# Performance work log

Measured on AMD Instinct MI355X. Metric: run time of the kernel, lower is better.

Reference implementation:

```python
import jax, jax.numpy as jnp
import numpy as np

DELAY = 4
SKIP = 2
NF = 8
HS = 256
EPS = 1e-5


def setup_inputs() -> dict:
    key = jax.random.key(0)
    ks = jax.random.split(key, 11)
    B, NP, NO, T = 16, 512, 512, 2048
    predictor = jax.random.normal(ks[0], (B, NP, T), dtype=jnp.float32)
    to_order = jax.random.normal(ks[1], (B, NO, T), dtype=jnp.float32)
    trilinear = jax.random.normal(ks[2], (NF, NO, NP), dtype=jnp.float32) / np.float32(np.sqrt(NP * NO))
    w_o = jax.random.normal(ks[3], (HS, NO), dtype=jnp.float32) / np.float32(np.sqrt(NO))
    b_o = jax.random.normal(ks[4], (HS,), dtype=jnp.float32) * 0.01
    w_p = jax.random.normal(ks[5], (HS, NP), dtype=jnp.float32) / np.float32(np.sqrt(NP))
    b_p = jax.random.normal(ks[6], (HS,), dtype=jnp.float32) * 0.01
    bn_gamma = jnp.ones((HS,), dtype=jnp.float32)
    bn_beta = jnp.zeros((HS,), dtype=jnp.float32)
    w_out = jax.random.normal(ks[7], (NF, HS), dtype=jnp.float32) / np.float32(np.sqrt(HS))
    b_out = jax.random.normal(ks[8], (NF,), dtype=jnp.float32) * 0.01
    return {"predictor": predictor, "to_order": to_order, "trilinear": trilinear,
            "w_o": w_o, "b_o": b_o, "w_p": w_p, "b_p": b_p,
            "bn_gamma": bn_gamma, "bn_beta": bn_beta, "w_out": w_out, "b_out": b_out}


def reference(predictor, to_order, trilinear, w_o, b_o, w_p, b_p, bn_gamma, bn_beta, w_out, b_out):
    B, NP, T = predictor.shape
    NO = to_order.shape[1]
    tot_latency = DELAY + SKIP * (NF - 1)
    T_r = T - tot_latency
    pred = predictor[:, :, :T_r]          # (B, np, Tr)
    too = to_order[:, :, DELAY:]          # (B, no, T - delay)
    # predictor_product[b,k,t,m] = sum_p pred[b,p,t] * trilinear[k,m,p]
    pp = jnp.einsum('bpt,kmp->bktm', pred, trilinear)           # (B, nf, Tr, no)
    win = jnp.stack([too[:, :, j * SKIP: j * SKIP + T_r] for j in range(NF)], axis=1)  # (B, nf, no, Tr)
    inner = jnp.einsum('bjmt,bktm->bjkt', win, pp)              # (B, nf, nf, Tr)
    # conv1d (kernel 1) heads
    o_proj = jnp.einsum('hm,bmt->bht', w_o, too) + b_o[None, :, None]    # (B, hs, T - delay)
    p_proj = jnp.einsum('hp,bpt->bht', w_p, pred) + b_p[None, :, None]   # (B, hs, Tr)
    o_win = jnp.stack([o_proj[:, :, j * SKIP: j * SKIP + T_r] for j in range(NF)], axis=1)  # (B, nf, hs, Tr)
    h = jax.nn.relu(o_win + p_proj[:, None])                    # (B, nf, hs, Tr)
    # BatchNorm1d (training-mode batch stats) over (B*nf, hs, Tr): stats over axes (0,1,3)
    mean = h.mean(axis=(0, 1, 3), keepdims=True)
    var = h.var(axis=(0, 1, 3), keepdims=True)
    h = (h - mean) * jax.lax.rsqrt(var + EPS) * bn_gamma[None, None, :, None] + bn_beta[None, None, :, None]
    head = jnp.einsum('kh,bjht->bjkt', w_out, h) + b_out[None, None, :, None]
    inner = inner + head
    log_probs = jax.nn.log_softmax(inner, axis=2)               # (B, nf, nf, Tr)
    correct = jnp.einsum('bjjt->bjt', log_probs)                # diagonal j == k
    return correct.mean(axis=2).mean(axis=0)                    # (nf,)
```

## Files before the change

### kernel.cpp

```cpp
#include <hip/hip_runtime.h>
#include <math.h>

constexpr int B_  = 16;
constexpr int NP_ = 512;
constexpr int NO_ = 512;
constexpr int T_  = 2048;
constexpr int NF_ = 8;
constexpr int HS_ = 256;
constexpr int TR_ = 2030;
constexpr int TO_ = 2044;
constexpr int OPLD_ = 2048;
constexpr float EPS_ = 1e-5f;

typedef short bf16x8 __attribute__((ext_vector_type(8)));
typedef float f32x16 __attribute__((ext_vector_type(16)));

__device__ __forceinline__ unsigned short f2bf(float f) {
  union { float f; unsigned int u; } v; v.f = f;
  unsigned int r = v.u + 0x7fffu + ((v.u >> 16) & 1u);
  return (unsigned short)(r >> 16);
}
__device__ __forceinline__ float bf2f(unsigned short u) {
  union { unsigned int u; float f; } v; v.u = ((unsigned int)u) << 16;
  return v.f;
}

typedef const __attribute__((address_space(1))) unsigned int* gas_u32;
typedef __attribute__((address_space(3))) unsigned int* las_u32;
__device__ __forceinline__ void gl16(const void* g, void* l) {
  __builtin_amdgcn_global_load_lds((gas_u32)g, (las_u32)l, 16, 0, 0);
}


__global__ __launch_bounds__(256) void transpose_cvt(
    const float* __restrict__ in, unsigned short* __restrict__ outb) {
  __shared__ float tile[64][65];
  const int c0 = blockIdx.x * 64;
  const int r0 = blockIdx.y * 64;
  const int b  = blockIdx.z;
  const float* ib = in + (size_t)b * 512 * 2048;
  unsigned short* ob = outb + (size_t)b * 2048 * 512;
  for (int i = threadIdx.x; i < 64 * 16; i += 256) {
    const int r = i >> 4, c4 = (i & 15) * 4;
    float4 v = *(const float4*)(ib + (size_t)(r0 + r) * 2048 + c0 + c4);
    tile[r][c4 + 0] = v.x; tile[r][c4 + 1] = v.y;
    tile[r][c4 + 2] = v.z; tile[r][c4 + 3] = v.w;
  }
  __syncthreads();
  for (int i = threadIdx.x; i < 64 * 8; i += 256) {
    const int c = i >> 3, r8 = (i & 7) * 8;
    unsigned int pk[4];
    #pragma unroll
    for (int e = 0; e < 4; ++e)
      pk[e] = (unsigned int)f2bf(tile[r8 + 2 * e][c]) |
              ((unsigned int)f2bf(tile[r8 + 2 * e + 1][c]) << 16);
    *(uint4*)(ob + (size_t)(c0 + c) * 512 + r0 + r8) = *(uint4*)pk;
  }
}

__global__ __launch_bounds__(256) void cvt_bf16(
    const float* __restrict__ in, unsigned short* __restrict__ out, int n) {
  const int i = (blockIdx.x * 256 + threadIdx.x) * 4;
  if (i < n) {
    float4 v = *(const float4*)(in + i);
    ushort4 o; o.x = f2bf(v.x); o.y = f2bf(v.y); o.z = f2bf(v.z); o.w = f2bf(v.w);
    *(ushort4*)(out + i) = o;
  }
}

__global__ __launch_bounds__(256, 2) void proj_mfma(
    const unsigned short* __restrict__ Wbf,
    const unsigned short* __restrict__ Xt,
    const float* __restrict__ bias,
    unsigned short* __restrict__ out,
    int Tlen, int toff) {
  __shared__ char smem[65536];
  char* const Ab[2] = { smem, smem + 16384 };
  char* const Bb[2] = { smem + 32768, smem + 49152 };
  const int tid = threadIdx.x;
  const int l = tid & 63, wv = tid >> 6;
  const int h = l >> 5, tl = l & 31;
  const int mq = wv >> 1, tq = wv & 1;
  const int t0 = blockIdx.x * 128;
  const int m0 = blockIdx.y * 128;
  const int b  = blockIdx.z;
  const unsigned short* Xb = Xt + (size_t)b * T_ * 512;

  int aSrc[4], bSrc[4], ldsO[4];
  #pragma unroll
  for (int i = 0; i < 4; ++i) {
    const int q = (wv << 8) + (i << 6) + l;
    const int r = q >> 3, c8s = (q & 7) ^ (r & 7);
    aSrc[i] = (m0 + r) * 512 + (c8s << 3);
    const int row = min(t0 + toff + r, T_ - 1);
    bSrc[i] = row * 512 + (c8s << 3);
    ldsO[i] = ((wv << 8) + (i << 6)) << 4;
  }

  f32x16 acc[2][2];
  #pragma unroll
  for (int i = 0; i < 2; ++i)
    #pragma unroll
    for (int jj = 0; jj < 2; ++jj)
      #pragma unroll
      for (int e = 0; e < 16; ++e) acc[i][jj][e] = 0.f;

  #pragma unroll
  for (int i = 0; i < 4; ++i) gl16(Wbf + aSrc[i], Ab[0] + ldsO[i]);
  #pragma unroll
  for (int i = 0; i < 4; ++i) gl16(Xb + bSrc[i], Bb[0] + ldsO[i]);
  asm volatile("s_waitcnt vmcnt(0)" ::: "memory");
  __builtin_amdgcn_s_barrier();

  #pragma unroll
  for (int ps = 0; ps < 8; ++ps) {
    const int cb = ps & 1;
    if (ps < 7) {
      const int p0 = (ps + 1) << 6;
      #pragma unroll
      for (int i = 0; i < 4; ++i) gl16(Wbf + p0 + aSrc[i], Ab[cb ^ 1] + ldsO[i]);
      #pragma unroll
      for (int i = 0; i < 4; ++i) gl16(Xb + p0 + bSrc[i], Bb[cb ^ 1] + ldsO[i]);
    }
    const unsigned short* As = (const unsigned short*)Ab[cb];
    const unsigned short* Bs = (const unsigned short*)Bb[cb];
    #pragma unroll
    for (int s = 0; s < 4; ++s) {
      const int k8 = 2 * s + h;
      bf16x8 af[2], bfr[2];
      #pragma unroll
      for (int mt = 0; mt < 2; ++mt) {
        const int rm = 64 * mq + 32 * mt + tl;
        af[mt] = *(const bf16x8*)(As + rm * 64 + ((k8 ^ (rm & 7)) << 3));
      }
      #pragma unroll
      for (int nt = 0; nt < 2; ++nt) {
        const int rt = 64 * tq + 32 * nt + tl;
        bfr[nt] = *(const bf16x8*)(Bs + rt * 64 + ((k8 ^ (rt & 7)) << 3));
      }
      #pragma unroll
      for (int mt = 0; mt < 2; ++mt)
        #pragma unroll
        for (int nt = 0; nt < 2; ++nt)
          acc[mt][nt] = __builtin_amdgcn_mfma_f32_32x32x16_bf16(
              af[mt], bfr[nt], acc[mt][nt], 0, 0, 0);
    }
    asm volatile("s_waitcnt vmcnt(0)" ::: "memory");
    __builtin_amdgcn_s_barrier();
  }
  #pragma unroll
  for (int mt = 0; mt < 2; ++mt)
    #pragma unroll
    for (int nt = 0; nt < 2; ++nt)
      #pragma unroll
      for (int r = 0; r < 16; ++r) {
        const int hs = m0 + 64 * mq + 32 * mt + (r & 3) + 8 * (r >> 2) + 4 * h;
        const int t  = t0 + 64 * tq + 32 * nt + tl;
        if (t < Tlen)
          out[((size_t)b * HS_ + hs) * OPLD_ + t] = f2bf(acc[mt][nt][r] + bias[hs]);
      }
}

__global__ __launch_bounds__(256, 2) void inner_mfma(
    const unsigned short* __restrict__ pred_t,
    const unsigned short* __restrict__ too_t,
    const unsigned short* __restrict__ tri_bf,
    float* __restrict__ inner) {
  __shared__ char smem[69632];
  char* const Pb[2] = { smem, smem + 16384 };
  char* const Tb[2] = { smem + 32768, smem + 40960 };
  char* const TOO   = smem + 49152;
  const int tid = threadIdx.x;
  const int l = tid & 63, wv = tid >> 6;
  const int h = l >> 5, tl = l & 31;
  const int t0 = blockIdx.x * 128;
  const int kf = blockIdx.y;
  const int b  = blockIdx.z;
  const unsigned short* predB = pred_t + (size_t)b * T_ * NP_;
  const unsigned short* tooB  = too_t  + (size_t)b * T_ * NO_;
  const unsigned short* triK  = tri_bf + (size_t)kf * NO_ * NP_;

  int pSrc[4], pLds[4];
  #pragma unroll
  for (int i = 0; i < 4; ++i) {
    const int q = (wv << 8) + (i << 6) + l;
    const int r = q >> 3, c8s = (q & 7) ^ (r & 7);
    pSrc[i] = (t0 + r) * NP_ + (c8s << 3);
    pLds[i] = ((wv << 8) + (i << 6)) << 4;
  }
  int tSrc[2], tLds[2];
  #pragma unroll
  for (int i = 0; i < 2; ++i) {
    const int q = (wv << 7) + (i << 6) + l;
    const int r = q >> 3, c8s = (q & 7) ^ (r & 7);
    tSrc[i] = r * NP_ + (c8s << 3);
    tLds[i] = ((wv << 7) + (i << 6)) << 4;
  }
  int oSrc[5], oLds[5];
  #pragma unroll
  for (int i = 0; i < 5; ++i) {
    const int q = wv * 320 + (i << 6) + l;
    const int r = q >> 3, c8s = (q & 7) ^ (r & 7);
    const int row = min(t0 + r, T_ - 1);
    oSrc[i] = row * NO_ + (c8s << 3);
    oLds[i] = (wv * 320 + (i << 6)) << 4;
  }

  f32x16 Sacc[2];
  #pragma unroll
  for (int ct = 0; ct < 2; ++ct)
    #pragma unroll
    for (int e = 0; e < 16; ++e) Sacc[ct][e] = 0.f;

  for (int mc = 0; mc < 8; ++mc) {
    const int m0 = mc << 6;
    const int mOff = m0 * NP_;
    __builtin_amdgcn_s_barrier();
    #pragma unroll
    for (int i = 0; i < 5; ++i) gl16(tooB + m0 + oSrc[i], TOO + oLds[i]);
    #pragma unroll
    for (int i = 0; i < 4; ++i) gl16(predB + pSrc[i], Pb[0] + pLds[i]);
    #pragma unroll
    for (int i = 0; i < 2; ++i) gl16(triK + mOff + tSrc[i], Tb[0] + tLds[i]);
    asm volatile("s_waitcnt vmcnt(0)" ::: "memory");
    __builtin_amdgcn_s_barrier();

    f32x16 Qacc[2];
    #pragma unroll
    for (int mt = 0; mt < 2; ++mt)
      #pragma unroll
      for (int e = 0; e < 16; ++e) Qacc[mt][e] = 0.f;

    #pragma unroll
    for (int ps = 0; ps < 8; ++ps) {
      const int cb = ps & 1;
      if (ps < 7) {
        const int p0 = (ps + 1) << 6;
        #pragma unroll
        for (int i = 0; i < 4; ++i) gl16(predB + p0 + pSrc[i], Pb[cb ^ 1] + pLds[i]);
        #pragma unroll
        for (int i = 0; i < 2; ++i) gl16(triK + mOff + p0 + tSrc[i], Tb[cb ^ 1] + tLds[i]);
      }
      const unsigned short* predS = (const unsigned short*)Pb[cb];
      const unsigned short* triS  = (const unsigned short*)Tb[cb];
      #pragma unroll
      for (int s = 0; s < 4; ++s) {
        const int k8 = 2 * s + h;
        const int rb = (wv << 5) + tl;
        const bf16x8 bp = *(const bf16x8*)(predS + rb * 64 + ((k8 ^ (rb & 7)) << 3));
        #pragma unroll
        for (int mt = 0; mt < 2; ++mt) {
          const int rm = (mt << 5) + tl;
          const bf16x8 at = *(const bf16x8*)(triS + rm * 64 + ((k8 ^ (rm & 7)) << 3));
          Qacc[mt] = __builtin_amdgcn_mfma_f32_32x32x16_bf16(at, bp, Qacc[mt], 0, 0, 0);
        }
      }
      asm volatile("s_waitcnt vmcnt(0)" ::: "memory");
      __builtin_amdgcn_s_barrier();
    }
    unsigned short* QSw = (unsigned short*)(Pb[0] + (wv << 12));
    #pragma unroll
    for (int mt = 0; mt < 2; ++mt)
      #pragma unroll
      for (int rp = 0; rp < 8; ++rp) {
        const int r = rp << 1;
        const int m = (mt << 5) + (r & 3) + ((r >> 2) << 3) + (h << 2);
        const int c8 = m >> 3, ml = m & 7;
        const int rX = (tl & 24) | ((tl ^ c8) & 7);
        const unsigned int pk = (unsigned int)f2bf(Qacc[mt][r]) |
                                ((unsigned int)f2bf(Qacc[mt][r + 1]) << 16);
        *(unsigned int*)(QSw + (((c8 << 5) + rX) << 3) + ml) = pk;
      }
    const unsigned short* tooS = (const unsigned short*)TOO;
    #pragma unroll
    for (int s = 0; s < 4; ++s) {
      const int k8 = 2 * s + h;
      const int rqX = (tl & 24) | ((tl ^ k8) & 7);
      const bf16x8 bq = *(const bf16x8*)(QSw + (((k8 << 5) + rqX) << 3));
      #pragma unroll
      for (int ct = 0; ct < 2; ++ct) {
        const int rr = (wv << 5) + (ct << 5) + tl;
        const bf16x8 atoo = *(const bf16x8*)(tooS + rr * 64 + ((k8 ^ (rr & 7)) << 3));
        Sacc[ct] = __builtin_amdgcn_mfma_f32_32x32x16_bf16(atoo, bq, Sacc[ct], 0, 0, 0);
      }
    }
  }
  __syncthreads();
  float* SW = (float*)smem + (wv << 11);
  #pragma unroll
  for (int ct = 0; ct < 2; ++ct)
    #pragma unroll
    for (int r = 0; r < 16; ++r) {
      const int cc = (ct << 5) + (r & 3) + ((r >> 2) << 3) + (h << 2);
      SW[(cc << 5) + tl] = Sacc[ct][r];
    }
  const int tglob = t0 + (wv << 5) + tl;
  if (tglob < TR_) {
    #pragma unroll
    for (int jj = 0; jj < 4; ++jj) {
      const int j = (jj << 1) + h;
      const float v = SW[((tl + 4 + 2 * j) << 5) + tl];
      inner[(((size_t)b * NF_ + j) * NF_ + kf) * TR_ + tglob] = v;
    }
  }
}

__global__ __launch_bounds__(256) void bn_stats(
    const unsigned short* __restrict__ op, const unsigned short* __restrict__ pp,
    float* __restrict__ partials) {
  const int hh = blockIdx.x, b = blockIdx.y;
  const unsigned short* oprow = op + ((size_t)b * HS_ + hh) * OPLD_;
  const unsigned short* pprow = pp + ((size_t)b * HS_ + hh) * OPLD_;
  float s = 0.f, s2 = 0.f;
  for (int t = threadIdx.x; t < TR_; t += 256) {
    const float pv = bf2f(pprow[t]);
    #pragma unroll
    for (int j = 0; j < NF_; ++j) {
      float r = bf2f(oprow[t + 2 * j]) + pv;
      r = fmaxf(r, 0.f);
      s += r; s2 += r * r;
    }
  }
  __shared__ float red[256], red2[256];
  red[threadIdx.x] = s; red2[threadIdx.x] = s2;
  __syncthreads();
  for (int st = 128; st > 0; st >>= 1) {
    if (threadIdx.x < st) {
      red[threadIdx.x]  += red[threadIdx.x + st];
      red2[threadIdx.x] += red2[threadIdx.x + st];
    }
    __syncthreads();
  }
  if (threadIdx.x == 0) {
    partials[b * HS_ + hh]            = red[0];
    partials[B_ * HS_ + b * HS_ + hh] = red2[0];
  }
}

__global__ __launch_bounds__(256) void bn_finalize(
    const float* __restrict__ partials, const float* __restrict__ gamma,
    const float* __restrict__ beta, const float* __restrict__ w_out,
    const float* __restrict__ b_out, float* __restrict__ w_eff,
    float* __restrict__ cvec) {
  const int hh = threadIdx.x;
  float s = 0.f, s2 = 0.f;
  for (int b = 0; b < B_; ++b) {
    s  += partials[b * HS_ + hh];
    s2 += partials[B_ * HS_ + b * HS_ + hh];
  }
  const float cnt  = (float)B_ * NF_ * TR_;
  const float mean = s / cnt;
  const float var  = s2 / cnt - mean * mean;
  const float scale = gamma[hh] * rsqrtf(var + EPS_);
  const float shift = beta[hh] - mean * scale;
  #pragma unroll
  for (int k = 0; k < NF_; ++k) w_eff[k * HS_ + hh] = w_out[k * HS_ + hh] * scale;
  __shared__ float red[256];
  for (int k = 0; k < NF_; ++k) {
    red[hh] = w_out[k * HS_ + hh] * shift;
    __syncthreads();
    for (int st = 128; st > 0; st >>= 1) {
      if (hh < st) red[hh] += red[hh + st];
      __syncthreads();
    }
    if (hh == 0) cvec[k] = b_out[k] + red[0];
    __syncthreads();
  }
}

__global__ __launch_bounds__(256) void head_final(
    const unsigned short* __restrict__ op, const unsigned short* __restrict__ pp,
    const float* __restrict__ w_eff, const float* __restrict__ cvec,
    const float* __restrict__ inner, float* __restrict__ part3) {
  __shared__ float opS[288 * 20];
  __shared__ float ppS[256 * 20];
  __shared__ float weS[8][256];
  __shared__ float red[4][5];
  const int tid = threadIdx.x;
  const int t0 = blockIdx.x * 256;
  const int b  = blockIdx.y;
  const int jh = blockIdx.z;
  for (int i = tid; i < 8 * 256; i += 256) weS[i >> 8][i & 255] = w_eff[i];
  float acc[4][8] = {};
  const unsigned short* opb = op + (size_t)b * HS_ * OPLD_;
  const unsigned short* ppb = pp + (size_t)b * HS_ * OPLD_;
  for (int hc = 0; hc < 16; ++hc) {
    const int h0 = hc << 4;
    __syncthreads();
    for (int idx = tid; idx < 576; idx += 256) {
      const int r = idx / 36, cc = (idx - r * 36) << 3;
      const int g = min(t0 + cc, OPLD_ - 8);
      uint4 v = *(const uint4*)(opb + (size_t)(h0 + r) * OPLD_ + g);
      #pragma unroll
      for (int e = 0; e < 4; ++e) {
        const unsigned int u = (&v.x)[e];
        opS[(cc + 2 * e) * 20 + r]     = bf2f((unsigned short)(u & 0xffffu));
        opS[(cc + 2 * e + 1) * 20 + r] = bf2f((unsigned short)(u >> 16));
      }
    }
    for (int idx = tid; idx < 512; idx += 256) {
      const int r = idx >> 5, cc = (idx & 31) << 3;
      uint4 v = *(const uint4*)(ppb + (size_t)(h0 + r) * OPLD_ + t0 + cc);
      #pragma unroll
      for (int e = 0; e < 4; ++e) {
        const unsigned int u = (&v.x)[e];
        ppS[(cc + 2 * e) * 20 + r]     = bf2f((unsigned short)(u & 0xffffu));
        ppS[(cc + 2 * e + 1) * 20 + r] = bf2f((unsigned short)(u >> 16));
      }
    }
    __syncthreads();
    float pv[16];
    #pragma unroll
    for (int i = 0; i < 4; ++i) {
      float4 q = *(const float4*)(ppS + tid * 20 + 4 * i);
      pv[4 * i + 0] = q.x; pv[4 * i + 1] = q.y;
      pv[4 * i + 2] = q.z; pv[4 * i + 3] = q.w;
    }
    #pragma unroll
    for (int jj = 0; jj < 4; ++jj) {
      const int col = tid + 2 * ((jh << 2) + jj);
      #pragma unroll
      for (int i = 0; i < 4; ++i) {
        float4 ov = *(const float4*)(opS + col * 20 + 4 * i);
        #pragma unroll
        for (int e = 0; e < 4; ++e) {
          const float r = fmaxf((&ov.x)[e] + pv[4 * i + e], 0.f);
          #pragma unroll
          for (int k = 0; k < 8; ++k) acc[jj][k] += weS[k][h0 + 4 * i + e] * r;
        }
      }
    }
  }
  const int t = t0 + tid;
  float sj[4];
  #pragma unroll
  for (int jj = 0; jj < 4; ++jj) {
    if (t < TR_) {
      const int j = (jh << 2) + jj;
      float v[8]; float mx = -1e30f;
      #pragma unroll
      for (int k = 0; k < 8; ++k) {
        v[k] = acc[jj][k] + cvec[k] +
               inner[(((size_t)b * NF_ + j) * NF_ + k) * TR_ + t];
        mx = fmaxf(mx, v[k]);
      }
      float se = 0.f;
      #pragma unroll
      for (int k = 0; k < 8; ++k) se += expf(v[k] - mx);
      sj[jj] = v[j] - mx - logf(se);
    } else sj[jj] = 0.f;
  }
  #pragma unroll
  for (int jj = 0; jj < 4; ++jj)
    #pragma unroll
    for (int off = 32; off > 0; off >>= 1) sj[jj] += __shfl_down(sj[jj], off);
  if ((tid & 63) == 0) {
    const int wv = tid >> 6;
    #pragma unroll
    for (int jj = 0; jj < 4; ++jj) red[jj][wv] = sj[jj];
  }
  __syncthreads();
  if (tid < 4) {
    const float s = red[tid][0] + red[tid][1] + red[tid][2] + red[tid][3];
    const int j = (jh << 2) + tid;
    part3[(j * B_ + b) * 8 + blockIdx.x] = s;
  }
}

__global__ void final_out(const float* __restrict__ part3, float* __restrict__ out) {
  const int j = threadIdx.x;
  if (j < NF_) {
    float s = 0.f;
    for (int i = 0; i < B_ * 8; ++i) s += part3[j * B_ * 8 + i];
    out[j] = s / ((float)B_ * (float)TR_);
  }
}

extern "C" void kernel_launch(void* const* d_in, const int* in_sizes, int n_in,
                              void* d_out, int out_size, void* d_ws, size_t ws_size,
                              hipStream_t stream) {
  const float* predictor = (const float*)d_in[0];
  const float* to_order  = (const float*)d_in[1];
  const float* trilinear = (const float*)d_in[2];
  const float* w_o   = (const float*)d_in[3];
  const float* b_o   = (const float*)d_in[4];
  const float* w_p   = (const float*)d_in[5];
  const float* b_p   = (const float*)d_in[6];
  const float* bn_g  = (const float*)d_in[7];
  const float* bn_b  = (const float*)d_in[8];
  const float* w_out = (const float*)d_in[9];
  const float* b_out = (const float*)d_in[10];
  float* out = (float*)d_out;

  char* w = (char*)d_ws;
  unsigned short* pred_t = (unsigned short*)w; w += (size_t)B_ * T_ * NP_ * 2;
  unsigned short* too_t  = (unsigned short*)w; w += (size_t)B_ * T_ * NO_ * 2;
  unsigned short* tri_bf = (unsigned short*)w; w += (size_t)NF_ * NO_ * NP_ * 2;
  unsigned short* wo_bf  = (unsigned short*)w; w += (size_t)HS_ * NO_ * 2;
  unsigned short* wp_bf  = (unsigned short*)w; w += (size_t)HS_ * NP_ * 2;
  unsigned short* o_proj = (unsigned short*)w; w += (size_t)B_ * HS_ * OPLD_ * 2;
  unsigned short* p_proj = (unsigned short*)w; w += (size_t)B_ * HS_ * OPLD_ * 2;
  float* inner    = (float*)w; w += (size_t)B_ * NF_ * NF_ * TR_ * 4;
  float* partials = (float*)w; w += (size_t)2 * B_ * HS_ * 4;
  float* w_eff    = (float*)w; w += (size_t)NF_ * HS_ * 4;
  float* cvec     = (float*)w; w += 256;
  float* part3    = (float*)w; w += (size_t)NF_ * B_ * 8 * 4;

  transpose_cvt<<<dim3(32, 8, 16), 256, 0, stream>>>(predictor, pred_t);
  transpose_cvt<<<dim3(32, 8, 16), 256, 0, stream>>>(to_order, too_t);
  cvt_bf16<<<2048, 256, 0, stream>>>(trilinear, tri_bf, NF_ * NO_ * NP_);
  cvt_bf16<<<128, 256, 0, stream>>>(w_o, wo_bf, HS_ * NO_);
  cvt_bf16<<<128, 256, 0, stream>>>(w_p, wp_bf, HS_ * NP_);

  proj_mfma<<<dim3(16, 2, 16), 256, 0, stream>>>(wo_bf, too_t, b_o, o_proj, TO_, 4);
  proj_mfma<<<dim3(16, 2, 16), 256, 0, stream>>>(wp_bf, pred_t, b_p, p_proj, TR_, 0);

  inner_mfma<<<dim3(16, 8, 16), 256, 0, stream>>>(pred_t, too_t, tri_bf, inner);

  bn_stats<<<dim3(HS_, B_), 256, 0, stream>>>(o_proj, p_proj, partials);
  bn_finalize<<<1, 256, 0, stream>>>(partials, bn_g, bn_b, w_out, b_out, w_eff, cvec);
  head_final<<<dim3(8, B_, 2), 256, 0, stream>>>(o_proj, p_proj, w_eff, cvec, inner, part3);
  final_out<<<1, 64, 0, stream>>>(part3, out);
}
```

Measured before the change: 386.7 us.

## Enlarge inner_mfma tiles to two factors and 256 timesteps with deeper pipelining

Result: slower. 452.6 us (+17.1%).

```diff
diff --git a/kernel.cpp b/kernel.cpp
--- a/kernel.cpp
+++ b/kernel.cpp
@@ -161,146 +161,200 @@
       }
 }
 
-__global__ __launch_bounds__(256, 2) void inner_mfma(
+__global__ __launch_bounds__(512, 2) void inner_mfma(
     const unsigned short* __restrict__ pred_t,
     const unsigned short* __restrict__ too_t,
     const unsigned short* __restrict__ tri_bf,
     float* __restrict__ inner) {
-  __shared__ char smem[69632];
-  char* const Pb[2] = { smem, smem + 16384 };
-  char* const Tb[2] = { smem + 32768, smem + 40960 };
-  char* const TOO   = smem + 49152;
+  __shared__ char smem[159744];
   const int tid = threadIdx.x;
   const int l = tid & 63, wv = tid >> 6;
   const int h = l >> 5, tl = l & 31;
-  const int t0 = blockIdx.x * 128;
-  const int kf = blockIdx.y;
+  const int t0 = blockIdx.x * 256;
+  const int kf0 = blockIdx.y * 2;
   const int b  = blockIdx.z;
   const unsigned short* predB = pred_t + (size_t)b * T_ * NP_;
   const unsigned short* tooB  = too_t  + (size_t)b * T_ * NO_;
-  const unsigned short* triK  = tri_bf + (size_t)kf * NO_ * NP_;
-
-  int pSrc[4], pLds[4];
+  const unsigned short* triK  = tri_bf + (size_t)kf0 * NO_ * NP_;
+
+  char* const predW = smem + wv * 12288;
+  char* const triB0 = smem + 98304;
+  char* const tooS  = smem + 131072;
+
+  int pSrc[4];
   #pragma unroll
   for (int i = 0; i < 4; ++i) {
-    const int q = (wv << 8) + (i << 6) + l;
-    const int r = q >> 3, c8s = (q & 7) ^ (r & 7);
-    pSrc[i] = (t0 + r) * NP_ + (c8s << 3);
-    pLds[i] = ((wv << 8) + (i << 6)) << 4;
-  }
-  int tSrc[2], tLds[2];
+    const int q = (i << 6) + l;
+    const int rl = q >> 3, c8s = (q & 7) ^ (rl & 7);
+    pSrc[i] = (t0 + (wv << 5) + rl) * NP_ + (c8s << 3);
+  }
+  int tSrc[2];
   #pragma unroll
   for (int i = 0; i < 2; ++i) {
     const int q = (wv << 7) + (i << 6) + l;
+    const int f = q >> 9, qq = q & 511;
+    const int r = qq >> 3, c8s = (qq & 7) ^ (r & 7);
+    tSrc[i] = f * (NO_ * NP_) + r * NP_ + (c8s << 3);
+  }
+  int oSrc[4];
+  #pragma unroll
+  for (int i = 0; i < 4; ++i) {
+    const int q = (i < 3) ? (i * 512 + (wv << 6) + l) : (1536 + (wv << 6) + l);
     const int r = q >> 3, c8s = (q & 7) ^ (r & 7);
-    tSrc[i] = r * NP_ + (c8s << 3);
-    tLds[i] = ((wv << 7) + (i << 6)) << 4;
-  }
-  int oSrc[5], oLds[5];
-  #pragma unroll
-  for (int i = 0; i < 5; ++i) {
-    const int q = wv * 320 + (i << 6) + l;
-    const int r = q >> 3, c8s = (q & 7) ^ (r & 7);
-    const int row = min(t0 + r, T_ - 1);
-    oSrc[i] = row * NO_ + (c8s << 3);
-    oLds[i] = (wv * 320 + (i << 6)) << 4;
-  }
-
-  f32x16 Sacc[2];
-  #pragma unroll
-  for (int ct = 0; ct < 2; ++ct)
-    #pragma unroll
-    for (int e = 0; e < 16; ++e) Sacc[ct][e] = 0.f;
+    oSrc[i] = min(t0 + r, T_ - 1) * NO_ + (c8s << 3);
+  }
+
+  f32x16 Sacc[2][2];
+  #pragma unroll
+  for (int f = 0; f < 2; ++f)
+    #pragma unroll
+    for (int ct = 0; ct < 2; ++ct)
+      #pragma unroll
+      for (int e = 0; e < 16; ++e) Sacc[f][ct][e] = 0.f;
 
   for (int mc = 0; mc < 8; ++mc) {
     const int m0 = mc << 6;
     const int mOff = m0 * NP_;
     __builtin_amdgcn_s_barrier();
     #pragma unroll
-    for (int i = 0; i < 5; ++i) gl16(tooB + m0 + oSrc[i], TOO + oLds[i]);
-    #pragma unroll
-    for (int i = 0; i < 4; ++i) gl16(predB + pSrc[i], Pb[0] + pLds[i]);
-    #pragma unroll
-    for (int i = 0; i < 2; ++i) gl16(triK + mOff + tSrc[i], Tb[0] + tLds[i]);
-    asm volatile("s_waitcnt vmcnt(0)" ::: "memory");
-    __builtin_amdgcn_s_barrier();
-
-    f32x16 Qacc[2];
-    #pragma unroll
-    for (int mt = 0; mt < 2; ++mt)
-      #pragma unroll
-      for (int e = 0; e < 16; ++e) Qacc[mt][e] = 0.f;
+    for (int i = 0; i < 3; ++i)
+      gl16(tooB + m0 + oSrc[i], tooS + ((i * 512 + (wv << 6)) << 4));
+    if (wv < 4)
+      gl16(tooB + m0 + oSrc[3], tooS + ((1536 + (wv << 6)) << 4));
+    #pragma unroll
+    for (int i = 0; i < 2; ++i)
+      gl16(triK + mOff + tSrc[i], triB0 + (((wv << 7) + (i << 6)) << 4));
+    #pragma unroll
+    for (int i = 0; i < 4; ++i) gl16(predB + pSrc[i], predW + (i << 10));
+    #pragma unroll
+    for (int i = 0; i < 4; ++i) gl16(predB + 64 + pSrc[i], predW + 4096 + (i << 10));
+
+    f32x16 Qacc[2][2];
+    #pragma unroll
+    for (int f = 0; f < 2; ++f)
+      #pragma unroll
+      for (int mt = 0; mt < 2; ++mt)
+        #pragma unroll
+        for (int e = 0; e < 16; ++e) Qacc[f][mt][e] = 0.f;
 
     #pragma unroll
     for (int ps = 0; ps < 8; ++ps) {
       const int cb = ps & 1;
+      const int pb = ps % 3;
+      if (ps < 7) asm volatile("s_waitcnt vmcnt(4)" ::: "memory");
+      else        asm volatile("s_waitcnt vmcnt(0)" ::: "memory");
+      __builtin_amdgcn_s_barrier();
       if (ps < 7) {
-        const int p0 = (ps + 1) << 6;
-        #pragma unroll
-        for (int i = 0; i < 4; ++i) gl16(predB + p0 + pSrc[i], Pb[cb ^ 1] + pLds[i]);
-        #pragma unroll
-        for (int i = 0; i < 2; ++i) gl16(triK + mOff + p0 + tSrc[i], Tb[cb ^ 1] + tLds[i]);
-      }
-      const unsigned short* predS = (const unsigned short*)Pb[cb];
-      const unsigned short* triS  = (const unsigned short*)Tb[cb];
+        const int p1 = (ps + 1) << 6;
+        #pragma unroll
+        for (int i = 0; i < 2; ++i)
+          gl16(triK + mOff + p1 + tSrc[i],
+               triB0 + (cb ^ 1) * 16384 + (((wv << 7) + (i << 6)) << 4));
+      }
+      if (ps < 6) {
+        const int p2 = (ps + 2) << 6;
+        const int pb2 = (ps + 2) % 3;
+        #pragma unroll
+        for (int i = 0; i < 4; ++i)
+          gl16(predB + p2 + pSrc[i], predW + pb2 * 4096 + (i << 10));
+      }
+      if (ps == 7) {
+        if (wv == 6) {
+          #pragma unroll
+          for (int i = 0; i < 4; ++i) {
+            const int q = (i << 6) + l;
+            const int r = 224 + (q >> 3), c8s = (q & 7) ^ (r & 7);
+            gl16(tooB + m0 + min(t0 + r, T_ - 1) * NO_ + (c8s << 3),
+                 triB0 + (i << 10));
+          }
+        } else if (wv == 7) {
+          #pragma unroll
+          for (int i = 0; i < 8; ++i) {
+            const int q = (i << 6) + l;
+            const int r = 224 + (q >> 3), c8s = (q & 7) ^ (r & 7);
+            gl16(tooB + m0 + min(t0 + r, T_ - 1) * NO_ + (c8s << 3),
+                 triB0 + 4096 + (i << 10));
+          }
+        }
+      }
+      const char* triS0 = triB0 + cb * 16384;
+      const char* triS1 = triS0 + 8192;
+      const char* ppS   = predW + pb * 4096;
+      __builtin_amdgcn_s_setprio(1);
       #pragma unroll
       for (int s = 0; s < 4; ++s) {
         const int k8 = 2 * s + h;
-        const int rb = (wv << 5) + tl;
-        const bf16x8 bp = *(const bf16x8*)(predS + rb * 64 + ((k8 ^ (rb & 7)) << 3));
+        const bf16x8 bp = *(const bf16x8*)(ppS + (((tl << 3) + (k8 ^ (tl & 7))) << 4));
         #pragma unroll
         for (int mt = 0; mt < 2; ++mt) {
           const int rm = (mt << 5) + tl;
-          const bf16x8 at = *(const bf16x8*)(triS + rm * 64 + ((k8 ^ (rm & 7)) << 3));
-          Qacc[mt] = __builtin_amdgcn_mfma_f32_32x32x16_bf16(at, bp, Qacc[mt], 0, 0, 0);
+          const int co = ((rm << 3) + (k8 ^ (tl & 7))) << 4;
+          const bf16x8 a0 = *(const bf16x8*)(triS0 + co);
+          const bf16x8 a1 = *(const bf16x8*)(triS1 + co);
+          Qacc[0][mt] = __builtin_amdgcn_mfma_f32_32x32x16_bf16(a0, bp, Qacc[0][mt], 0, 0, 0);
+          Qacc[1][mt] = __builtin_amdgcn_mfma_f32_32x32x16_bf16(a1, bp, Qacc[1][mt], 0, 0, 0);
         }
       }
-      asm volatile("s_waitcnt vmcnt(0)" ::: "memory");
-      __builtin_amdgcn_s_barrier();
-    }
-    unsigned short* QSw = (unsigned short*)(Pb[0] + (wv << 12));
-    #pragma unroll
-    for (int mt = 0; mt < 2; ++mt)
-      #pragma unroll
-      for (int rp = 0; rp < 8; ++rp) {
-        const int r = rp << 1;
-        const int m = (mt << 5) + (r & 3) + ((r >> 2) << 3) + (h << 2);
-        const int c8 = m >> 3, ml = m & 7;
-        const int rX = (tl & 24) | ((tl ^ c8) & 7);
-        const unsigned int pk = (unsigned int)f2bf(Qacc[mt][r]) |
-                                ((unsigned int)f2bf(Qacc[mt][r + 1]) << 16);
-        *(unsigned int*)(QSw + (((c8 << 5) + rX) << 3) + ml) = pk;
-      }
-    const unsigned short* tooS = (const unsigned short*)TOO;
+      __builtin_amdgcn_s_setprio(0);
+    }
+    asm volatile("s_waitcnt vmcnt(0)" ::: "memory");
+    #pragma unroll
+    for (int f = 0; f < 2; ++f) {
+      unsigned short* QSw = (unsigned short*)(predW + (f << 12));
+      #pragma unroll
+      for (int mt = 0; mt < 2; ++mt)
+        #pragma unroll
+        for (int rp = 0; rp < 8; ++rp) {
+          const int r = rp << 1;
+          const int m = (mt << 5) + (r & 3) + ((r >> 2) << 3) + (h << 2);
+          const int c8 = m >> 3, ml = m & 7;
+          const int rX = (tl & 24) | ((tl ^ c8) & 7);
+          const unsigned int pk = (unsigned int)f2bf(Qacc[f][mt][r]) |
+                                  ((unsigned int)f2bf(Qacc[f][mt][r + 1]) << 16);
+          *(unsigned int*)(QSw + (((c8 << 5) + rX) << 3) + ml) = pk;
+        }
+    }
     #pragma unroll
     for (int s = 0; s < 4; ++s) {
       const int k8 = 2 * s + h;
+      bf16x8 atoo[2];
+      #pragma unroll
+      for (int ct = 0; ct < 2; ++ct) {
+        const int rbase = (wv << 5) + (ct << 5);
+        const char* tb = (rbase < 224)
+            ? (tooS + rbase * 128)
+            : (triB0 + ((wv == 7) ? 4096 : 0) + (rbase - 224) * 128);
+        atoo[ct] = *(const bf16x8*)(tb + tl * 128 + ((k8 ^ (tl & 7)) << 4));
+      }
       const int rqX = (tl & 24) | ((tl ^ k8) & 7);
-      const bf16x8 bq = *(const bf16x8*)(QSw + (((k8 << 5) + rqX) << 3));
-      #pragma unroll
-      for (int ct = 0; ct < 2; ++ct) {
-        const int rr = (wv << 5) + (ct << 5) + tl;
-        const bf16x8 atoo = *(const bf16x8*)(tooS + rr * 64 + ((k8 ^ (rr & 7)) << 3));
-        Sacc[ct] = __builtin_amdgcn_mfma_f32_32x32x16_bf16(atoo, bq, Sacc[ct], 0, 0, 0);
-      }
-    }
-  }
-  __syncthreads();
-  float* SW = (float*)smem + (wv << 11);
-  #pragma unroll
-  for (int ct = 0; ct < 2; ++ct)
-    #pragma unroll
-    for (int r = 0; r < 16; ++r) {
-      const int cc = (ct << 5) + (r & 3) + ((r >> 2) << 3) + (h << 2);
-      SW[(cc << 5) + tl] = Sacc[ct][r];
-    }
+      #pragma unroll
+      for (int f = 0; f < 2; ++f) {
+        const bf16x8 bq = *(const bf16x8*)((const unsigned short*)(predW + (f << 12)) +
+                                           (((k8 << 5) + rqX) << 3));
+        #pragma unroll
+        for (int ct = 0; ct < 2; ++ct)
+          Sacc[f][ct] = __builtin_amdgcn_mfma_f32_32x32x16_bf16(atoo[ct], bq, Sacc[f][ct], 0, 0, 0);
+      }
+    }
+  }
   const int tglob = t0 + (wv << 5) + tl;
-  if (tglob < TR_) {
-    #pragma unroll
-    for (int jj = 0; jj < 4; ++jj) {
-      const int j = (jj << 1) + h;
-      const float v = SW[((tl + 4 + 2 * j) << 5) + tl];
-      inner[(((size_t)b * NF_ + j) * NF_ + kf) * TR_ + tglob] = v;
+  float* SW = (float*)predW;
+  #pragma unroll
+  for (int f = 0; f < 2; ++f) {
+    #pragma unroll
+    for (int ct = 0; ct < 2; ++ct)
+      #pragma unroll
+      for (int r = 0; r < 16; ++r) {
+        const int cc = (ct << 5) + (r & 3) + ((r >> 2) << 3) + (h << 2);
+        SW[(cc << 5) + tl] = Sacc[f][ct][r];
+      }
+    if (tglob < TR_) {
+      #pragma unroll
+      for (int jj = 0; jj < 4; ++jj) {
+        const int j = (jj << 1) + h;
+        const float v = SW[((tl + 4 + 2 * j) << 5) + tl];
+        inner[(((size_t)b * NF_ + j) * NF_ + (kf0 + f)) * TR_ + tglob] = v;
+      }
     }
   }
 }
@@ -515,7 +569,7 @@
   proj_mfma<<<dim3(16, 2, 16), 256, 0, stream>>>(wo_bf, too_t, b_o, o_proj, TO_, 4);
   proj_mfma<<<dim3(16, 2, 16), 256, 0, stream>>>(wp_bf, pred_t, b_p, p_proj, TR_, 0);
 
-  inner_mfma<<<dim3(16, 8, 16), 256, 0, stream>>>(pred_t, too_t, tri_bf, inner);
+  inner_mfma<<<dim3(8, 4, 16), 512, 0, stream>>>(pred_t, too_t, tri_bf, inner);
 
   bn_stats<<<dim3(HS_, B_), 256, 0, stream>>>(o_proj, p_proj, partials);
   bn_finalize<<<1, 256, 0, stream>>>(partials, bn_g, bn_b, w_out, b_out, w_eff, cvec);
```

## Process two trilinear factors per inner_mfma block to reuse predictor and too tiles

Applied to the files above, without the earlier changes.

Measured after the change: 338.2 us. -12.5%, faster.

```diff
diff --git a/kernel.cpp b/kernel.cpp
--- a/kernel.cpp
+++ b/kernel.cpp
@@ -166,19 +166,20 @@
     const unsigned short* __restrict__ too_t,
     const unsigned short* __restrict__ tri_bf,
     float* __restrict__ inner) {
-  __shared__ char smem[69632];
+  __shared__ char smem[77824];
   char* const Pb[2] = { smem, smem + 16384 };
-  char* const Tb[2] = { smem + 32768, smem + 40960 };
-  char* const TOO   = smem + 49152;
+  char* const Tb[2] = { smem + 32768, smem + 49152 };
+  char* const TOOM  = smem + 65536;
+  char* const TAIL  = smem + 32768;
   const int tid = threadIdx.x;
   const int l = tid & 63, wv = tid >> 6;
   const int h = l >> 5, tl = l & 31;
   const int t0 = blockIdx.x * 128;
-  const int kf = blockIdx.y;
+  const int kf0 = blockIdx.y * 2;
   const int b  = blockIdx.z;
   const unsigned short* predB = pred_t + (size_t)b * T_ * NP_;
   const unsigned short* tooB  = too_t  + (size_t)b * T_ * NO_;
-  const unsigned short* triK  = tri_bf + (size_t)kf * NO_ * NP_;
+  const unsigned short* triK  = tri_bf + (size_t)kf0 * NO_ * NP_;
 
   int pSrc[4], pLds[4];
   #pragma unroll
@@ -188,58 +189,75 @@
     pSrc[i] = (t0 + r) * NP_ + (c8s << 3);
     pLds[i] = ((wv << 8) + (i << 6)) << 4;
   }
-  int tSrc[2], tLds[2];
-  #pragma unroll
-  for (int i = 0; i < 2; ++i) {
-    const int q = (wv << 7) + (i << 6) + l;
+  int tSrc[4], tLds[4];
+  #pragma unroll
+  for (int i = 0; i < 4; ++i) {
+    const int q = (wv << 8) + (i << 6) + l;
+    const int f = q >> 9, qq = q & 511;
+    const int r = qq >> 3, c8s = (qq & 7) ^ (r & 7);
+    tSrc[i] = f * (NO_ * NP_) + r * NP_ + (c8s << 3);
+    tLds[i] = ((wv << 8) + (i << 6)) << 4;
+  }
+  int oSrc[3], oLds[3];
+  #pragma unroll
+  for (int i = 0; i < 3; ++i) {
+    const int q = wv * 192 + (i << 6) + l;
     const int r = q >> 3, c8s = (q & 7) ^ (r & 7);
-    tSrc[i] = r * NP_ + (c8s << 3);
-    tLds[i] = ((wv << 7) + (i << 6)) << 4;
-  }
-  int oSrc[5], oLds[5];
-  #pragma unroll
-  for (int i = 0; i < 5; ++i) {
-    const int q = wv * 320 + (i << 6) + l;
-    const int r = q >> 3, c8s = (q & 7) ^ (r & 7);
-    const int row = min(t0 + r, T_ - 1);
-    oSrc[i] = row * NO_ + (c8s << 3);
-    oLds[i] = (wv * 320 + (i << 6)) << 4;
-  }
-
-  f32x16 Sacc[2];
-  #pragma unroll
-  for (int ct = 0; ct < 2; ++ct)
-    #pragma unroll
-    for (int e = 0; e < 16; ++e) Sacc[ct][e] = 0.f;
+    oSrc[i] = (t0 + r) * NO_ + (c8s << 3);
+    oLds[i] = (wv * 192 + (i << 6)) << 4;
+  }
+  int aSrcT[4], aLdsT[4];
+  {
+    const int ws = (wv >= 2) ? (wv - 2) : 0;
+    #pragma unroll
+    for (int i = 0; i < 4; ++i) {
+      const int q = (ws << 8) + (i << 6) + l;
+      const int r = 96 + (q >> 3), c8s = (q & 7) ^ (r & 7);
+      aSrcT[i] = min(t0 + r, T_ - 1) * NO_ + (c8s << 3);
+      aLdsT[i] = ((ws << 8) + (i << 6)) << 4;
+    }
+  }
+
+  f32x16 Sacc[2][2];
+  #pragma unroll
+  for (int f = 0; f < 2; ++f)
+    #pragma unroll
+    for (int ct = 0; ct < 2; ++ct)
+      #pragma unroll
+      for (int e = 0; e < 16; ++e) Sacc[f][ct][e] = 0.f;
 
   for (int mc = 0; mc < 8; ++mc) {
     const int m0 = mc << 6;
     const int mOff = m0 * NP_;
     __builtin_amdgcn_s_barrier();
     #pragma unroll
-    for (int i = 0; i < 5; ++i) gl16(tooB + m0 + oSrc[i], TOO + oLds[i]);
+    for (int i = 0; i < 3; ++i) gl16(tooB + m0 + oSrc[i], TOOM + oLds[i]);
+    #pragma unroll
+    for (int i = 0; i < 4; ++i) gl16(triK + mOff + tSrc[i], Tb[0] + tLds[i]);
     #pragma unroll
     for (int i = 0; i < 4; ++i) gl16(predB + pSrc[i], Pb[0] + pLds[i]);
-    #pragma unroll
-    for (int i = 0; i < 2; ++i) gl16(triK + mOff + tSrc[i], Tb[0] + tLds[i]);
     asm volatile("s_waitcnt vmcnt(0)" ::: "memory");
     __builtin_amdgcn_s_barrier();
 
-    f32x16 Qacc[2];
-    #pragma unroll
-    for (int mt = 0; mt < 2; ++mt)
-      #pragma unroll
-      for (int e = 0; e < 16; ++e) Qacc[mt][e] = 0.f;
+    f32x16 Qacc[2][2];
+    #pragma unroll
+    for (int f = 0; f < 2; ++f)
+      #pragma unroll
+      for (int mt = 0; mt < 2; ++mt)
+        #pragma unroll
+        for (int e = 0; e < 16; ++e) Qacc[f][mt][e] = 0.f;
 
     #pragma unroll
     for (int ps = 0; ps < 8; ++ps) {
       const int cb = ps & 1;
       if (ps < 7) {
-        const int p0 = (ps + 1) << 6;
-        #pragma unroll
-        for (int i = 0; i < 4; ++i) gl16(predB + p0 + pSrc[i], Pb[cb ^ 1] + pLds[i]);
-        #pragma unroll
-        for (int i = 0; i < 2; ++i) gl16(triK + mOff + p0 + tSrc[i], Tb[cb ^ 1] + tLds[i]);
+        const int p1 = (ps + 1) << 6;
+        #pragma unroll
+        for (int i = 0; i < 4; ++i)
+          gl16(triK + mOff + p1 + tSrc[i], Tb[cb ^ 1] + tLds[i]);
+        #pragma unroll
+        for (int i = 0; i < 4; ++i)
+          gl16(predB + p1 + pSrc[i], Pb[cb ^ 1] + pLds[i]);
       }
       const unsigned short* predS = (const unsigned short*)Pb[cb];
       const unsigned short* triS  = (const unsigned short*)Tb[cb];
@@ -251,56 +269,80 @@
         #pragma unroll
         for (int mt = 0; mt < 2; ++mt) {
           const int rm = (mt << 5) + tl;
-          const bf16x8 at = *(const bf16x8*)(triS + rm * 64 + ((k8 ^ (rm & 7)) << 3));
-          Qacc[mt] = __builtin_amdgcn_mfma_f32_32x32x16_bf16(at, bp, Qacc[mt], 0, 0, 0);
+          const int co = rm * 64 + ((k8 ^ (rm & 7)) << 3);
+          const bf16x8 a0 = *(const bf16x8*)(triS + co);
+          const bf16x8 a1 = *(const bf16x8*)(triS + 2048 + co);
+          Qacc[0][mt] = __builtin_amdgcn_mfma_f32_32x32x16_bf16(a0, bp, Qacc[0][mt], 0, 0, 0);
+          Qacc[1][mt] = __builtin_amdgcn_mfma_f32_32x32x16_bf16(a1, bp, Qacc[1][mt], 0, 0, 0);
         }
+      }
+      if (ps == 7 && wv >= 2) {
+        #pragma unroll
+        for (int i = 0; i < 4; ++i)
+          gl16(tooB + m0 + aSrcT[i], TAIL + aLdsT[i]);
       }
       asm volatile("s_waitcnt vmcnt(0)" ::: "memory");
       __builtin_amdgcn_s_barrier();
     }
-    unsigned short* QSw = (unsigned short*)(Pb[0] + (wv << 12));
-    #pragma unroll
-    for (int mt = 0; mt < 2; ++mt)
-      #pragma unroll
-      for (int rp = 0; rp < 8; ++rp) {
-        const int r = rp << 1;
-        const int m = (mt << 5) + (r & 3) + ((r >> 2) << 3) + (h << 2);
-        const int c8 = m >> 3, ml = m & 7;
-        const int rX = (tl & 24) | ((tl ^ c8) & 7);
-        const unsigned int pk = (unsigned int)f2bf(Qacc[mt][r]) |
-                                ((unsigned int)f2bf(Qacc[mt][r + 1]) << 16);
-        *(unsigned int*)(QSw + (((c8 << 5) + rX) << 3) + ml) = pk;
-      }
-    const unsigned short* tooS = (const unsigned short*)TOO;
+    #pragma unroll
+    for (int f = 0; f < 2; ++f) {
+      unsigned short* QSw = (unsigned short*)(Pb[f] + (wv << 12));
+      #pragma unroll
+      for (int mt = 0; mt < 2; ++mt)
+        #pragma unroll
+        for (int rp = 0; rp < 8; ++rp) {
+          const int r = rp << 1;
+          const int m = (mt << 5) + (r & 3) + ((r >> 2) << 3) + (h << 2);
+          const int c8 = m >> 3, ml = m & 7;
+          const int rX = (tl & 24) | ((tl ^ c8) & 7);
+          const unsigned int pk = (unsigned int)f2bf(Qacc[f][mt][r]) |
+                                  ((unsigned int)f2bf(Qacc[f][mt][r + 1]) << 16);
+          *(unsigned int*)(QSw + (((c8 << 5) + rX) << 3) + ml) = pk;
+        }
+    }
     #pragma unroll
     for (int s = 0; s < 4; ++s) {
       const int k8 = 2 * s + h;
+      bf16x8 atoo[2];
+      #pragma unroll
+      for (int ct = 0; ct < 2; ++ct) {
+        const int rbase = (wv + ct) << 5;
+        const int rr = rbase + tl;
+        const unsigned short* tb = (rbase < 96)
+            ? (const unsigned short*)TOOM + (size_t)rr * 64
+            : (const unsigned short*)TAIL + (size_t)(rr - 96) * 64;
+        atoo[ct] = *(const bf16x8*)(tb + ((k8 ^ (rr & 7)) << 3));
+      }
       const int rqX = (tl & 24) | ((tl ^ k8) & 7);
-      const bf16x8 bq = *(const bf16x8*)(QSw + (((k8 << 5) + rqX) << 3));
-      #pragma unroll
-      for (int ct = 0; ct < 2; ++ct) {
-        const int rr = (wv << 5) + (ct << 5) + tl;
-        const bf16x8 atoo = *(const bf16x8*)(tooS + rr * 64 + ((k8 ^ (rr & 7)) << 3));
-        Sacc[ct] = __builtin_amdgcn_mfma_f32_32x32x16_bf16(atoo, bq, Sacc[ct], 0, 0, 0);
+      #pragma unroll
+      for (int f = 0; f < 2; ++f) {
+        const bf16x8 bq = *(const bf16x8*)((const unsigned short*)(Pb[f] + (wv << 12)) +
+                                           (((k8 << 5) + rqX) << 3));
+        #pragma unroll
+        for (int ct = 0; ct < 2; ++ct)
+          Sacc[f][ct] = __builtin_amdgcn_mfma_f32_32x32x16_bf16(atoo[ct], bq, Sacc[f][ct], 0, 0, 0);
       }
     }
   }
   __syncthreads();
+  const int tglob = t0 + (wv << 5) + tl;
   float* SW = (float*)smem + (wv << 11);
   #pragma unroll
-  for (int ct = 0; ct < 2; ++ct)
-    #pragma unroll
-    for (int r = 0; r < 16; ++r) {
-      const int cc = (ct << 5) + (r & 3) + ((r >> 2) << 3) + (h << 2);
-      SW[(cc << 5) + tl] = Sacc[ct][r];
-    }
-  const int tglob = t0 + (wv << 5) + tl;
-  if (tglob < TR_) {
-    #pragma unroll
-    for (int jj = 0; jj < 4; ++jj) {
-      const int j = (jj << 1) + h;
-      const float v = SW[((tl + 4 + 2 * j) << 5) + tl];
-      inner[(((size_t)b * NF_ + j) * NF_ + kf) * TR_ + tglob] = v;
+  for (int f = 0; f < 2; ++f) {
+    #pragma unroll
+    for (int ct = 0; ct < 2; ++ct)
+      #pragma unroll
+      for (int r = 0; r < 16; ++r) {
+        const int cc = (ct << 5) + (r & 3) + ((r >> 2) << 3) + (h << 2);
+        SW[(cc << 5) + tl] = Sacc[f][ct][r];
+      }
+    if (tglob < TR_) {
+      #pragma unroll
+      for (int jj = 0; jj < 4; ++jj) {
+        const int j = (jj << 1) + h;
+        const float v = SW[((tl + 4 + 2 * j) << 5) + tl];
+        inner[(((size_t)b * NF_ + j) * NF_ + (kf0 + f)) * TR_ + tglob] = v;
+      }
     }
   }
 }
@@ -515,7 +557,7 @@
   proj_mfma<<<dim3(16, 2, 16), 256, 0, stream>>>(wo_bf, too_t, b_o, o_proj, TO_, 4);
   proj_mfma<<<dim3(16, 2, 16), 256, 0, stream>>>(wp_bf, pred_t, b_p, p_proj, TR_, 0);
 
-  inner_mfma<<<dim3(16, 8, 16), 256, 0, stream>>>(pred_t, too_t, tri_bf, inner);
+  inner_mfma<<<dim3(16, 4, 16), 256, 0, stream>>>(pred_t, too_t, tri_bf, inner);
 
   bn_stats<<<dim3(HS_, B_), 256, 0, stream>>>(o_proj, p_proj, partials);
   bn_finalize<<<1, 256, 0, stream>>>(partials, bn_g, bn_b, w_out, b_out, w_eff, cvec);
```
